# Kernel tuning notes

Measured on AMD Instinct MI355X. Metric: run time of the kernel, lower is better.

## Reference

```python
import jax, jax.numpy as jnp
import numpy as np

N_NODES = 100000
N_EDGES = 3200000
D_IN, D_HID, D_OUT = 128, 128, 128


def setup_inputs() -> dict:
    key = jax.random.key(0)
    ks = jax.random.split(key, 8)
    x = jax.random.normal(ks[0], (N_NODES, D_IN), dtype=jnp.float32)
    edge_index = jax.random.randint(ks[1], (2, N_EDGES), 0, N_NODES, dtype=jnp.int64)
    def lin(k, din, dout):
        # glorot-ish init for GCNConv weight
        s = 1.0 / np.sqrt(din)
        return jax.random.uniform(k, (din, dout), jnp.float32, -s, s)
    W0 = lin(ks[2], D_IN, D_HID)
    b0 = jnp.zeros((D_HID,), jnp.float32)
    W1 = lin(ks[3], D_HID, D_HID)
    b1 = jnp.zeros((D_HID,), jnp.float32)
    W2 = lin(ks[4], D_HID, D_OUT)
    b2 = jnp.zeros((D_OUT,), jnp.float32)
    return {"x": x, "edge_index": edge_index, "W0": W0, "b0": b0,
            "W1": W1, "b1": b1, "W2": W2, "b2": b2}


def _gcn_norm(edge_index, n_nodes):
    # PyG gcn_norm with self-loops: deg over target index, sym normalization
    loop = jnp.arange(n_nodes, dtype=edge_index.dtype)
    src = jnp.concatenate([edge_index[0], loop])
    dst = jnp.concatenate([edge_index[1], loop])
    deg = jax.ops.segment_sum(jnp.ones_like(dst, dtype=jnp.float32), dst,
                              num_segments=n_nodes)
    dinv = jnp.where(deg > 0, jax.lax.rsqrt(deg), 0.0)
    norm = dinv[src] * dinv[dst]  # [E + N]
    return src, dst, norm


def _gcn_conv(h, src, dst, norm, W, b, n_nodes):
    h = h @ W                                   # [N, dout] transform first
    msg = h[src] * norm[:, None]                # gather + scale
    out = jax.ops.segment_sum(msg, dst, num_segments=n_nodes)  # scatter-add
    return out + b


def reference(x, edge_index, W0, b0, W1, b1, W2, b2):
    n = x.shape[0]
    src, dst, norm = _gcn_norm(edge_index, n)
    # layer 0
    h = jax.nn.relu(_gcn_conv(x, src, dst, norm, W0, b0, n))
    # residual middle layer (dropout is identity in eval mode)
    h = jax.nn.relu(_gcn_conv(h, src, dst, norm, W1, b1, n) + h)
    # output layer
    return _gcn_conv(h, src, dst, norm, W2, b2, n)
```

## Files before the change

### kernel.cpp

```cpp
#include <hip/hip_runtime.h>
#include <hip/hip_fp16.h>

#define D 128
typedef unsigned long long ull;
typedef _Float16 half8 __attribute__((ext_vector_type(8)));
typedef _Float16 half4v __attribute__((ext_vector_type(4)));
typedef float f32x4 __attribute__((ext_vector_type(4)));

#define KPOS(k4) (((k4) & ~31) + ((((k4) & 15) >> 2) << 3) + ((((k4) >> 4) & 1) << 2))

__global__ void k_zero_int(int* p, int n) {
  int i = blockIdx.x * blockDim.x + threadIdx.x;
  if (i < n) p[i] = 0;
}

__global__ void k_deg_count(const int* __restrict__ ei, int* __restrict__ deg, int E) {
  int e = blockIdx.x * blockDim.x + threadIdx.x;
  if (e < E) atomicAdd(&deg[ei[E + e]], 1);
}

__global__ void k_scan_part(const int* __restrict__ deg, int* __restrict__ part, int n) {
  __shared__ int sd[256];
  int base = blockIdx.x * 2048 + threadIdx.x * 8;
  int s = 0;
#pragma unroll
  for (int k = 0; k < 8; k++) {
    int idx = base + k;
    if (idx < n) s += deg[idx];
  }
  sd[threadIdx.x] = s;
  __syncthreads();
  for (int off = 128; off > 0; off >>= 1) {
    if (threadIdx.x < off) sd[threadIdx.x] += sd[threadIdx.x + off];
    __syncthreads();
  }
  if (threadIdx.x == 0) part[blockIdx.x] = sd[0];
}

__global__ void k_scan_offsets(int* __restrict__ part, int nparts,
                               int* __restrict__ rowptr, int n) {
  __shared__ int sd[256];
  int v = (threadIdx.x < nparts) ? part[threadIdx.x] : 0;
  sd[threadIdx.x] = v;
  __syncthreads();
  for (int off = 1; off < 256; off <<= 1) {
    int t = (threadIdx.x >= off) ? sd[threadIdx.x - off] : 0;
    __syncthreads();
    sd[threadIdx.x] += t;
    __syncthreads();
  }
  if (threadIdx.x < nparts) part[threadIdx.x] = sd[threadIdx.x] - v;
  if (threadIdx.x == 0) rowptr[n] = sd[255];
}

__global__ void k_scan_final(const int* __restrict__ deg, const int* __restrict__ part,
                             int* __restrict__ rowptr, int n) {
  __shared__ int sd[256];
  int base = blockIdx.x * 2048 + threadIdx.x * 8;
  int loc[8];
  int s = 0;
#pragma unroll
  for (int k = 0; k < 8; k++) {
    int idx = base + k;
    loc[k] = (idx < n) ? deg[idx] : 0;
    s += loc[k];
  }
  sd[threadIdx.x] = s;
  __syncthreads();
  for (int off = 1; off < 256; off <<= 1) {
    int t = (threadIdx.x >= off) ? sd[threadIdx.x - off] : 0;
    __syncthreads();
    sd[threadIdx.x] += t;
    __syncthreads();
  }
  int run = part[blockIdx.x] + sd[threadIdx.x] - s;
#pragma unroll
  for (int k = 0; k < 8; k++) {
    int idx = base + k;
    if (idx < n) {
      rowptr[idx] = run;
      run += loc[k];
    }
  }
}

__global__ void k_dinv_cursor(const int* __restrict__ rowptr, float* __restrict__ dinv,
                              int* __restrict__ cursor, int n) {
  int i = blockIdx.x * blockDim.x + threadIdx.x;
  if (i < n) {
    int r0 = rowptr[i], r1 = rowptr[i + 1];
    dinv[i] = rsqrtf((float)(r1 - r0) + 1.0f);
    cursor[i] = r0;
  }
}

__global__ void k_csr_fill_b(const int* __restrict__ ei, int* __restrict__ cursor,
                             int* __restrict__ csr, int E, int lo, int hi) {
  int e = blockIdx.x * blockDim.x + threadIdx.x;
  if (e >= E) return;
  int d = __builtin_nontemporal_load(&ei[E + e]);
  if (d < lo || d >= hi) return;
  int s = __builtin_nontemporal_load(&ei[e]);
  int pos = atomicAdd(&cursor[d], 1);
  csr[pos] = s;
}

template <int HALF_IN>
__launch_bounds__(256, 2)
__global__ void k_gemm_mfma(const void* __restrict__ Av, const float* __restrict__ W,
                            const float* __restrict__ dinv, __half* __restrict__ Th, int n) {
  __shared__ _Float16 Al[128 * 136];
  __shared__ _Float16 Bl[128 * 136];
  const int tid = threadIdx.x;
  const int row0 = blockIdx.x * 128;

  if (HALF_IN) {
    const _Float16* A = (const _Float16*)Av;
    for (int i = tid; i < 2048; i += 256) {
      int r = i >> 4;
      int k8 = (i & 15) << 3;
      half8 v = {0, 0, 0, 0, 0, 0, 0, 0};
      if (row0 + r < n) v = *(const half8*)&A[(size_t)(row0 + r) * D + k8];
      *(half4v*)&Al[r * 136 + KPOS(k8)]     = (half4v){v[0], v[1], v[2], v[3]};
      *(half4v*)&Al[r * 136 + KPOS(k8 + 4)] = (half4v){v[4], v[5], v[6], v[7]};
    }
  } else {
    const float* A = (const float*)Av;
    for (int i = tid; i < 4096; i += 256) {
      int r = i >> 5;
      int k4 = (i & 31) << 2;
      float4 v = make_float4(0.f, 0.f, 0.f, 0.f);
      if (row0 + r < n) v = ((const float4*)A)[(size_t)(row0 + r) * 32 + (i & 31)];
      *(half4v*)&Al[r * 136 + KPOS(k4)] =
          (half4v){(_Float16)v.x, (_Float16)v.y, (_Float16)v.z, (_Float16)v.w};
    }
  }
  for (int i = tid; i < 4096; i += 256) {
    int c = i & 127;
    int k4 = (i >> 7) << 2;
    float w0 = W[(k4 + 0) * D + c];
    float w1 = W[(k4 + 1) * D + c];
    float w2 = W[(k4 + 2) * D + c];
    float w3 = W[(k4 + 3) * D + c];
    *(half4v*)&Bl[c * 136 + KPOS(k4)] =
        (half4v){(_Float16)w0, (_Float16)w1, (_Float16)w2, (_Float16)w3};
  }
  __syncthreads();

  const int w = tid >> 6;
  const int lane = tid & 63;
  const int g = lane >> 4;
  const int q = lane & 15;

  f32x4 acc[2][8];
#pragma unroll
  for (int mt = 0; mt < 2; mt++)
#pragma unroll
    for (int nt = 0; nt < 8; nt++) acc[mt][nt] = (f32x4){0.f, 0.f, 0.f, 0.f};

#pragma unroll
  for (int kt = 0; kt < 4; kt++) {
    half8 a[2], b[8];
#pragma unroll
    for (int mt = 0; mt < 2; mt++)
      a[mt] = *(const half8*)&Al[(w * 32 + mt * 16 + q) * 136 + kt * 32 + g * 8];
#pragma unroll
    for (int nt = 0; nt < 8; nt++)
      b[nt] = *(const half8*)&Bl[(nt * 16 + q) * 136 + kt * 32 + g * 8];
#pragma unroll
    for (int mt = 0; mt < 2; mt++)
#pragma unroll
      for (int nt = 0; nt < 8; nt++)
        acc[mt][nt] = __builtin_amdgcn_mfma_f32_16x16x32_f16(a[mt], b[nt], acc[mt][nt], 0, 0, 0);
  }

#pragma unroll
  for (int mt = 0; mt < 2; mt++) {
    int baseRow = row0 + w * 32 + mt * 16 + g * 4;
    float dv[4];
#pragma unroll
    for (int r = 0; r < 4; r++) dv[r] = (baseRow + r < n) ? dinv[baseRow + r] : 0.f;
#pragma unroll
    for (int nt = 0; nt < 8; nt++) {
      int col = nt * 16 + q;
#pragma unroll
      for (int r = 0; r < 4; r++) {
        int gr = baseRow + r;
        if (gr < n) Th[(size_t)gr * D + col] = (__half)(acc[mt][nt][r] * dv[r]);
      }
    }
  }
}

template <int MODE>
__launch_bounds__(256)
__global__ void k_aggregate(const int* __restrict__ rowptr, const int* __restrict__ csr,
                            const float* __restrict__ dinv, const __half* __restrict__ th,
                            const float* __restrict__ b, const __half* __restrict__ resh,
                            __half* __restrict__ outh, float* __restrict__ outf, int n) {
  int node = blockIdx.x * 16 + (threadIdx.x >> 4);
  if (node >= n) return;
  const int l16 = threadIdx.x & 15;

  int beg = rowptr[node];
  int end = rowptr[node + 1];
  float dd = dinv[node];

  const float4* t4 = (const float4*)th;

  float a0, a1, a2, a3, a4, a5, a6, a7;
  {
    float4 raw = t4[(size_t)node * 16 + l16];
    const __half2* hp = (const __half2*)&raw;
    float2 f0 = __half22float2(hp[0]);
    float2 f1 = __half22float2(hp[1]);
    float2 f2 = __half22float2(hp[2]);
    float2 f3 = __half22float2(hp[3]);
    a0 = f0.x; a1 = f0.y; a2 = f1.x; a3 = f1.y;
    a4 = f2.x; a5 = f2.y; a6 = f3.x; a7 = f3.y;
  }

#define ACC_ROW(raw)                                  \
  {                                                   \
    const __half2* hp = (const __half2*)&(raw);       \
    float2 f0 = __half22float2(hp[0]);                \
    float2 f1 = __half22float2(hp[1]);                \
    float2 f2 = __half22float2(hp[2]);                \
    float2 f3 = __half22float2(hp[3]);                \
    a0 += f0.x; a1 += f0.y; a2 += f1.x; a3 += f1.y;   \
    a4 += f2.x; a5 += f2.y; a6 += f3.x; a7 += f3.y;   \
  }

  int j = beg;
  for (; j + 8 <= end; j += 8) {
    float4 r0, r1, r2, r3, r4, r5, r6, r7;
    {
      int s0 = __builtin_nontemporal_load(&csr[j + 0]);
      int s1 = __builtin_nontemporal_load(&csr[j + 1]);
      int s2 = __builtin_nontemporal_load(&csr[j + 2]);
      int s3 = __builtin_nontemporal_load(&csr[j + 3]);
      int s4 = __builtin_nontemporal_load(&csr[j + 4]);
      int s5 = __builtin_nontemporal_load(&csr[j + 5]);
      int s6 = __builtin_nontemporal_load(&csr[j + 6]);
      int s7 = __builtin_nontemporal_load(&csr[j + 7]);
      r0 = t4[(size_t)(unsigned)s0 * 16 + l16];
      r1 = t4[(size_t)(unsigned)s1 * 16 + l16];
      r2 = t4[(size_t)(unsigned)s2 * 16 + l16];
      r3 = t4[(size_t)(unsigned)s3 * 16 + l16];
      r4 = t4[(size_t)(unsigned)s4 * 16 + l16];
      r5 = t4[(size_t)(unsigned)s5 * 16 + l16];
      r6 = t4[(size_t)(unsigned)s6 * 16 + l16];
      r7 = t4[(size_t)(unsigned)s7 * 16 + l16];
    }
    ACC_ROW(r0) ACC_ROW(r1) ACC_ROW(r2) ACC_ROW(r3)
    ACC_ROW(r4) ACC_ROW(r5) ACC_ROW(r6) ACC_ROW(r7)
  }
  for (; j + 4 <= end; j += 4) {
    int s0 = __builtin_nontemporal_load(&csr[j + 0]);
    int s1 = __builtin_nontemporal_load(&csr[j + 1]);
    int s2 = __builtin_nontemporal_load(&csr[j + 2]);
    int s3 = __builtin_nontemporal_load(&csr[j + 3]);
    float4 r0 = t4[(size_t)(unsigned)s0 * 16 + l16];
    float4 r1 = t4[(size_t)(unsigned)s1 * 16 + l16];
    float4 r2 = t4[(size_t)(unsigned)s2 * 16 + l16];
    float4 r3 = t4[(size_t)(unsigned)s3 * 16 + l16];
    ACC_ROW(r0) ACC_ROW(r1) ACC_ROW(r2) ACC_ROW(r3)
  }
  for (; j < end; ++j) {
    int s = __builtin_nontemporal_load(&csr[j]);
    float4 r = t4[(size_t)(unsigned)s * 16 + l16];
    ACC_ROW(r)
  }
#undef ACC_ROW

  const float4* b4 = (const float4*)b;
  float4 bb0 = b4[l16 * 2];
  float4 bb1 = b4[l16 * 2 + 1];
  float o0 = fmaf(a0, dd, bb0.x), o1 = fmaf(a1, dd, bb0.y);
  float o2 = fmaf(a2, dd, bb0.z), o3 = fmaf(a3, dd, bb0.w);
  float o4 = fmaf(a4, dd, bb1.x), o5 = fmaf(a5, dd, bb1.y);
  float o6 = fmaf(a6, dd, bb1.z), o7 = fmaf(a7, dd, bb1.w);

  if (MODE == 1) {
    float4 raw = ((const float4*)resh)[(size_t)node * 16 + l16];
    const __half2* hp = (const __half2*)&raw;
    float2 f0 = __half22float2(hp[0]);
    float2 f1 = __half22float2(hp[1]);
    float2 f2 = __half22float2(hp[2]);
    float2 f3 = __half22float2(hp[3]);
    o0 += f0.x; o1 += f0.y; o2 += f1.x; o3 += f1.y;
    o4 += f2.x; o5 += f2.y; o6 += f3.x; o7 += f3.y;
  }
  if (MODE == 0 || MODE == 1) {
    o0 = fmaxf(o0, 0.f); o1 = fmaxf(o1, 0.f); o2 = fmaxf(o2, 0.f); o3 = fmaxf(o3, 0.f);
    o4 = fmaxf(o4, 0.f); o5 = fmaxf(o5, 0.f); o6 = fmaxf(o6, 0.f); o7 = fmaxf(o7, 0.f);
    union { __half2 h[4]; float4 f; } pk;
    pk.h[0] = __floats2half2_rn(o0, o1);
    pk.h[1] = __floats2half2_rn(o2, o3);
    pk.h[2] = __floats2half2_rn(o4, o5);
    pk.h[3] = __floats2half2_rn(o6, o7);
    ((float4*)outh)[(size_t)node * 16 + l16] = pk.f;
  } else {
    ((float4*)outf)[(size_t)node * 32 + l16 * 2] = make_float4(o0, o1, o2, o3);
    ((float4*)outf)[(size_t)node * 32 + l16 * 2 + 1] = make_float4(o4, o5, o6, o7);
  }
}

extern "C" void kernel_launch(void* const* d_in, const int* in_sizes, int n_in,
                              void* d_out, int out_size, void* d_ws, size_t ws_size,
                              hipStream_t stream) {
  const float* x  = (const float*)d_in[0];
  const int*   ei = (const int*)d_in[1];
  const float* W0 = (const float*)d_in[2];
  const float* b0 = (const float*)d_in[3];
  const float* W1 = (const float*)d_in[4];
  const float* b1 = (const float*)d_in[5];
  const float* W2 = (const float*)d_in[6];
  const float* b2 = (const float*)d_in[7];
  float* out = (float*)d_out;

  const int N = in_sizes[0] / D;
  const int E = in_sizes[1] / 2;

  char* wsb = (char*)d_ws;
  auto alloc = [&](size_t bytes) {
    char* p = wsb;
    wsb += ((bytes + 255) & ~(size_t)255);
    return p;
  };
  int*    rowptr = (int*)alloc((N + 1) * 4);
  int*    cursor = (int*)alloc(N * 4);
  int*    part   = (int*)alloc(256 * 4);
  float*  dinv   = (float*)alloc(N * 4);
  int*    csr    = (int*)alloc((size_t)E * 4);
  __half* th     = (__half*)alloc((size_t)N * D * 2);
  __half* g1h    = (__half*)alloc((size_t)N * D * 2);
  __half* g2h    = (__half*)alloc((size_t)N * D * 2);

  dim3 b256(256);
  int gN   = (N + 255) / 256;
  int gE   = (E + 255) / 256;
  int gGem = (N + 127) / 128;
  int gAgg = (N + 15) / 16;
  int nparts = (N + 2047) / 2048;

  int* deg = cursor;
  k_zero_int<<<gN, b256, 0, stream>>>(deg, N);
  k_deg_count<<<gE, b256, 0, stream>>>(ei, deg, E);
  k_scan_part<<<nparts, b256, 0, stream>>>(deg, part, N);
  k_scan_offsets<<<1, b256, 0, stream>>>(part, nparts, rowptr, N);
  k_scan_final<<<nparts, b256, 0, stream>>>(deg, part, rowptr, N);
  k_dinv_cursor<<<gN, b256, 0, stream>>>(rowptr, dinv, cursor, N);
  const int NB = 4;
  int bsz = (N + NB - 1) / NB;
  for (int b = 0; b < NB; b++) {
    int lo = b * bsz;
    int hi = lo + bsz;
    if (hi > N) hi = N;
    k_csr_fill_b<<<gE, b256, 0, stream>>>(ei, cursor, csr, E, lo, hi);
  }

  k_gemm_mfma<0><<<gGem, b256, 0, stream>>>(x, W0, dinv, th, N);
  k_aggregate<0><<<gAgg, b256, 0, stream>>>(rowptr, csr, dinv, th, b0, nullptr, g1h, nullptr, N);

  k_gemm_mfma<1><<<gGem, b256, 0, stream>>>(g1h, W1, dinv, th, N);
  k_aggregate<1><<<gAgg, b256, 0, stream>>>(rowptr, csr, dinv, th, b1, g1h, g2h, nullptr, N);

  k_gemm_mfma<1><<<gGem, b256, 0, stream>>>(g2h, W2, dinv, th, N);
  k_aggregate<2><<<gAgg, b256, 0, stream>>>(rowptr, csr, dinv, th, b2, nullptr, nullptr, out, N);
}
```

Baseline: 814.2 us.

## Privatize degree counts and fuse bucketed CSR fill into one launch

Degree counting now spreads atomics across 8 private copies of the degree array, chosen by block index, then reduces them in a separate pass, to cut same-address atomic contention. The four sequential bucketed CSR-fill launches become one persistent-style launch in which each block handles one of 8 destination buckets over a slice of edges. That removes launch gaps and lets the buckets run concurrently, while each bucket still confines its atomics to a narrower range of cursor addresses. The cost is an extra 8N-int buffer with its zeroing and reduction passes, and the edge list is still read once per bucket, now 8 times instead of 4.

```diff
diff --git a/kernel.cpp b/kernel.cpp
--- a/kernel.cpp
+++ b/kernel.cpp
@@ -14,9 +14,21 @@
   if (i < n) p[i] = 0;
 }
 
-__global__ void k_deg_count(const int* __restrict__ ei, int* __restrict__ deg, int E) {
+__global__ void k_deg_count8(const int* __restrict__ ei, int* __restrict__ deg8,
+                             int E, int N) {
   int e = blockIdx.x * blockDim.x + threadIdx.x;
-  if (e < E) atomicAdd(&deg[ei[E + e]], 1);
+  if (e >= E) return;
+  int d = __builtin_nontemporal_load(&ei[E + e]);
+  atomicAdd(&deg8[(blockIdx.x & 7) * N + d], 1);
+}
+
+__global__ void k_deg_reduce(const int* __restrict__ deg8, int* __restrict__ deg, int N) {
+  int i = blockIdx.x * blockDim.x + threadIdx.x;
+  if (i >= N) return;
+  int s = 0;
+#pragma unroll
+  for (int c = 0; c < 8; c++) s += deg8[c * N + i];
+  deg[i] = s;
 }
 
 __global__ void k_scan_part(const int* __restrict__ deg, int* __restrict__ part, int n) {
@@ -94,15 +106,24 @@
   }
 }
 
-__global__ void k_csr_fill_b(const int* __restrict__ ei, int* __restrict__ cursor,
-                             int* __restrict__ csr, int E, int lo, int hi) {
-  int e = blockIdx.x * blockDim.x + threadIdx.x;
-  if (e >= E) return;
-  int d = __builtin_nontemporal_load(&ei[E + e]);
-  if (d < lo || d >= hi) return;
-  int s = __builtin_nontemporal_load(&ei[e]);
-  int pos = atomicAdd(&cursor[d], 1);
-  csr[pos] = s;
+__global__ void k_csr_fill_x(const int* __restrict__ ei, int* __restrict__ cursor,
+                             int* __restrict__ csr, int E, int bsz) {
+  const int bucket = blockIdx.x & 7;
+  const int slice = blockIdx.x >> 3;
+  const int nsl = gridDim.x >> 3;
+  const int lo = bucket * bsz;
+  const int chunk = (E + nsl - 1) / nsl;
+  const int start = slice * chunk;
+  int endE = start + chunk;
+  if (endE > E) endE = E;
+  for (int e = start + threadIdx.x; e < endE; e += 256) {
+    int d = __builtin_nontemporal_load(&ei[E + e]);
+    if ((unsigned)(d - lo) < (unsigned)bsz) {
+      int s = __builtin_nontemporal_load(&ei[e]);
+      int pos = atomicAdd(&cursor[d], 1);
+      csr[pos] = s;
+    }
+  }
 }
 
 template <int HALF_IN>
@@ -332,6 +353,7 @@
   int*    cursor = (int*)alloc(N * 4);
   int*    part   = (int*)alloc(256 * 4);
   float*  dinv   = (float*)alloc(N * 4);
+  int*    deg8   = (int*)alloc((size_t)8 * N * 4);
   int*    csr    = (int*)alloc((size_t)E * 4);
   __half* th     = (__half*)alloc((size_t)N * D * 2);
   __half* g1h    = (__half*)alloc((size_t)N * D * 2);
@@ -339,26 +361,22 @@
 
   dim3 b256(256);
   int gN   = (N + 255) / 256;
+  int gN8  = (8 * N + 255) / 256;
   int gE   = (E + 255) / 256;
   int gGem = (N + 127) / 128;
   int gAgg = (N + 15) / 16;
   int nparts = (N + 2047) / 2048;
 
   int* deg = cursor;
-  k_zero_int<<<gN, b256, 0, stream>>>(deg, N);
-  k_deg_count<<<gE, b256, 0, stream>>>(ei, deg, E);
+  k_zero_int<<<gN8, b256, 0, stream>>>(deg8, 8 * N);
+  k_deg_count8<<<gE, b256, 0, stream>>>(ei, deg8, E, N);
+  k_deg_reduce<<<gN, b256, 0, stream>>>(deg8, deg, N);
   k_scan_part<<<nparts, b256, 0, stream>>>(deg, part, N);
   k_scan_offsets<<<1, b256, 0, stream>>>(part, nparts, rowptr, N);
   k_scan_final<<<nparts, b256, 0, stream>>>(deg, part, rowptr, N);
   k_dinv_cursor<<<gN, b256, 0, stream>>>(rowptr, dinv, cursor, N);
-  const int NB = 4;
-  int bsz = (N + NB - 1) / NB;
-  for (int b = 0; b < NB; b++) {
-    int lo = b * bsz;
-    int hi = lo + bsz;
-    if (hi > N) hi = N;
-    k_csr_fill_b<<<gE, b256, 0, stream>>>(ei, cursor, csr, E, lo, hi);
-  }
+  int bsz = (N + 7) / 8;
+  k_csr_fill_x<<<8 * 256, b256, 0, stream>>>(ei, cursor, csr, E, bsz);
 
   k_gemm_mfma<0><<<gGem, b256, 0, stream>>>(x, W0, dinv, th, N);
   k_aggregate<0><<<gAgg, b256, 0, stream>>>(rowptr, csr, dinv, th, b0, nullptr, g1h, nullptr, N);
```

Measured after the change: 746.3 us. 8.3% less time.

## Build CSR via two-level bucket sort with shared-memory atomics

Applied to the files above, without the earlier changes.

Replaces global-atomic degree counting and the four-pass filtered CSR fill with a bucketed counting sort. Edges are first histogrammed per tile into 512-node buckets, scattered into a bucket-ordered edge buffer, then each bucket computes degrees and fills CSR using shared-memory atomics. This is meant to remove the contended global atomics and the four repeated full reads of the edge list. In exchange it writes and reads an extra 8-byte-per-edge intermediate buffer and adds several kernel launches. Bucket count must stay at most 256 for the single-block scan, which holds for this node count.

```diff
diff --git a/kernel.cpp b/kernel.cpp
--- a/kernel.cpp
+++ b/kernel.cpp
@@ -2,6 +2,7 @@
 #include <hip/hip_fp16.h>
 
 #define D 128
+#define TILE 16384
 typedef unsigned long long ull;
 typedef _Float16 half8 __attribute__((ext_vector_type(8)));
 typedef _Float16 half4v __attribute__((ext_vector_type(4)));
@@ -9,24 +10,97 @@
 
 #define KPOS(k4) (((k4) & ~31) + ((((k4) & 15) >> 2) << 3) + ((((k4) >> 4) & 1) << 2))
 
-__global__ void k_zero_int(int* p, int n) {
-  int i = blockIdx.x * blockDim.x + threadIdx.x;
-  if (i < n) p[i] = 0;
-}
-
-__global__ void k_deg_count(const int* __restrict__ ei, int* __restrict__ deg, int E) {
-  int e = blockIdx.x * blockDim.x + threadIdx.x;
-  if (e < E) atomicAdd(&deg[ei[E + e]], 1);
-}
-
-__global__ void k_scan_part(const int* __restrict__ deg, int* __restrict__ part, int n) {
+__global__ void k_cnt_tiles(const int* __restrict__ ei_dst, int* __restrict__ cnt,
+                            int E, int ntiles, int nb) {
+  __shared__ int h[256];
+  for (int i = threadIdx.x; i < nb; i += 256) h[i] = 0;
+  __syncthreads();
+  const int t = blockIdx.x;
+  const int start = t * TILE;
+  int end = start + TILE;
+  if (end > E) end = E;
+  for (int i = start + threadIdx.x; i < end; i += 256)
+    atomicAdd(&h[__builtin_nontemporal_load(&ei_dst[i]) >> 9], 1);
+  __syncthreads();
+  for (int b = threadIdx.x; b < nb; b += 256)
+    cnt[(size_t)b * ntiles + t] = h[b];
+}
+
+__global__ void k_tile_scan(const int* __restrict__ cnt, int* __restrict__ off,
+                            int nb, int ntiles) {
   __shared__ int sd[256];
-  int base = blockIdx.x * 2048 + threadIdx.x * 8;
+  int total = 0;
+  if (threadIdx.x < nb) {
+    const int* row = cnt + (size_t)threadIdx.x * ntiles;
+    for (int t = 0; t < ntiles; t++) total += row[t];
+  }
+  sd[threadIdx.x] = total;
+  __syncthreads();
+  for (int o = 1; o < 256; o <<= 1) {
+    int v = (threadIdx.x >= o) ? sd[threadIdx.x - o] : 0;
+    __syncthreads();
+    sd[threadIdx.x] += v;
+    __syncthreads();
+  }
+  int base = sd[threadIdx.x] - total;
+  if (threadIdx.x < nb) {
+    const int* row = cnt + (size_t)threadIdx.x * ntiles;
+    int* orow = off + (size_t)threadIdx.x * ntiles;
+    int run = base;
+    for (int t = 0; t < ntiles; t++) { orow[t] = run; run += row[t]; }
+  }
+}
+
+__global__ void k_scatter_bucket(const int* __restrict__ ei, const int* __restrict__ off,
+                                 ull* __restrict__ ebb, int E, int ntiles, int nb) {
+  __shared__ int h[256];
+  __shared__ int base[256];
+  const int t = blockIdx.x;
+  for (int i = threadIdx.x; i < nb; i += 256) {
+    h[i] = 0;
+    base[i] = off[(size_t)i * ntiles + t];
+  }
+  __syncthreads();
+  const int start = t * TILE;
+  int end = start + TILE;
+  if (end > E) end = E;
+  for (int i = start + threadIdx.x; i < end; i += 256) {
+    int d = __builtin_nontemporal_load(&ei[E + i]);
+    int s = __builtin_nontemporal_load(&ei[i]);
+    int b = d >> 9;
+    int r = atomicAdd(&h[b], 1);
+    ebb[(size_t)base[b] + r] = (ull)(unsigned)s | ((ull)(unsigned)d << 32);
+  }
+}
+
+__global__ void k_deg_bucket(const ull* __restrict__ ebb, const int* __restrict__ off,
+                             int* __restrict__ deg, int E, int ntiles, int nb, int N) {
+  __shared__ int cnt[512];
+  const int b = blockIdx.x;
+  for (int i = threadIdx.x; i < 512; i += 256) cnt[i] = 0;
+  const int lo = off[(size_t)b * ntiles];
+  const int hi = (b + 1 < nb) ? off[(size_t)(b + 1) * ntiles] : E;
+  __syncthreads();
+  for (int i = lo + threadIdx.x; i < hi; i += 256) {
+    ull q = __builtin_nontemporal_load(&ebb[i]);
+    atomicAdd(&cnt[(int)(q >> 32) - (b << 9)], 1);
+  }
+  __syncthreads();
+  for (int i = threadIdx.x; i < 512; i += 256) {
+    int v = (b << 9) + i;
+    if (v < N) deg[v] = cnt[i];
+  }
+}
+
+template <int ITEMS>
+__global__ void k_scan_part(const int* __restrict__ v, int* __restrict__ part, int n) {
+  __shared__ int sd[256];
+  int base = blockIdx.x * (256 * ITEMS) + threadIdx.x * ITEMS;
   int s = 0;
 #pragma unroll
-  for (int k = 0; k < 8; k++) {
+  for (int k = 0; k < ITEMS; k++) {
     int idx = base + k;
-    if (idx < n) s += deg[idx];
+    if (idx < n) s += v[idx];
   }
   sd[threadIdx.x] = s;
   __syncthreads();
@@ -38,7 +112,7 @@
 }
 
 __global__ void k_scan_offsets(int* __restrict__ part, int nparts,
-                               int* __restrict__ rowptr, int n) {
+                               int* __restrict__ outp, int n) {
   __shared__ int sd[256];
   int v = (threadIdx.x < nparts) ? part[threadIdx.x] : 0;
   sd[threadIdx.x] = v;
@@ -50,19 +124,20 @@
     __syncthreads();
   }
   if (threadIdx.x < nparts) part[threadIdx.x] = sd[threadIdx.x] - v;
-  if (threadIdx.x == 0) rowptr[n] = sd[255];
-}
-
-__global__ void k_scan_final(const int* __restrict__ deg, const int* __restrict__ part,
-                             int* __restrict__ rowptr, int n) {
+  if (threadIdx.x == 0) outp[n] = sd[255];
+}
+
+template <int ITEMS>
+__global__ void k_scan_final(const int* __restrict__ v, const int* __restrict__ part,
+                             int* __restrict__ outp, int n) {
   __shared__ int sd[256];
-  int base = blockIdx.x * 2048 + threadIdx.x * 8;
-  int loc[8];
+  int base = blockIdx.x * (256 * ITEMS) + threadIdx.x * ITEMS;
+  int loc[ITEMS];
   int s = 0;
 #pragma unroll
-  for (int k = 0; k < 8; k++) {
+  for (int k = 0; k < ITEMS; k++) {
     int idx = base + k;
-    loc[k] = (idx < n) ? deg[idx] : 0;
+    loc[k] = (idx < n) ? v[idx] : 0;
     s += loc[k];
   }
   sd[threadIdx.x] = s;
@@ -75,34 +150,39 @@
   }
   int run = part[blockIdx.x] + sd[threadIdx.x] - s;
 #pragma unroll
-  for (int k = 0; k < 8; k++) {
+  for (int k = 0; k < ITEMS; k++) {
     int idx = base + k;
     if (idx < n) {
-      rowptr[idx] = run;
+      outp[idx] = run;
       run += loc[k];
     }
   }
 }
 
-__global__ void k_dinv_cursor(const int* __restrict__ rowptr, float* __restrict__ dinv,
-                              int* __restrict__ cursor, int n) {
+__global__ void k_dinv(const int* __restrict__ deg, float* __restrict__ dinv, int n) {
   int i = blockIdx.x * blockDim.x + threadIdx.x;
-  if (i < n) {
-    int r0 = rowptr[i], r1 = rowptr[i + 1];
-    dinv[i] = rsqrtf((float)(r1 - r0) + 1.0f);
-    cursor[i] = r0;
-  }
-}
-
-__global__ void k_csr_fill_b(const int* __restrict__ ei, int* __restrict__ cursor,
-                             int* __restrict__ csr, int E, int lo, int hi) {
-  int e = blockIdx.x * blockDim.x + threadIdx.x;
-  if (e >= E) return;
-  int d = __builtin_nontemporal_load(&ei[E + e]);
-  if (d < lo || d >= hi) return;
-  int s = __builtin_nontemporal_load(&ei[e]);
-  int pos = atomicAdd(&cursor[d], 1);
-  csr[pos] = s;
+  if (i < n) dinv[i] = rsqrtf((float)deg[i] + 1.0f);
+}
+
+__global__ void k_fill_bucket(const ull* __restrict__ ebb, const int* __restrict__ off,
+                              const int* __restrict__ rowptr, int* __restrict__ csr,
+                              int E, int ntiles, int nb, int N) {
+  __shared__ int cur[512];
+  const int b = blockIdx.x;
+  for (int i = threadIdx.x; i < 512; i += 256) {
+    int v = (b << 9) + i;
+    cur[i] = (v < N) ? rowptr[v] : 0;
+  }
+  const int lo = off[(size_t)b * ntiles];
+  const int hi = (b + 1 < nb) ? off[(size_t)(b + 1) * ntiles] : E;
+  __syncthreads();
+  for (int i = lo + threadIdx.x; i < hi; i += 256) {
+    ull q = __builtin_nontemporal_load(&ebb[i]);
+    int s = (int)(unsigned)q;
+    int dl = (int)(q >> 32) - (b << 9);
+    int pos = atomicAdd(&cur[dl], 1);
+    csr[pos] = s;
+  }
 }
 
 template <int HALF_IN>
@@ -322,6 +402,9 @@
   const int N = in_sizes[0] / D;
   const int E = in_sizes[1] / 2;
 
+  const int ntiles = (E + TILE - 1) / TILE;
+  const int nb = (N + 511) >> 9;
+
   char* wsb = (char*)d_ws;
   auto alloc = [&](size_t bytes) {
     char* p = wsb;
@@ -329,9 +412,12 @@
     return p;
   };
   int*    rowptr = (int*)alloc((N + 1) * 4);
-  int*    cursor = (int*)alloc(N * 4);
+  int*    deg    = (int*)alloc(N * 4);
   int*    part   = (int*)alloc(256 * 4);
   float*  dinv   = (float*)alloc(N * 4);
+  int*    cnt    = (int*)alloc((size_t)nb * ntiles * 4);
+  int*    off    = (int*)alloc((size_t)nb * ntiles * 4);
+  ull*    ebb    = (ull*)alloc((size_t)E * 8);
   int*    csr    = (int*)alloc((size_t)E * 4);
   __half* th     = (__half*)alloc((size_t)N * D * 2);
   __half* g1h    = (__half*)alloc((size_t)N * D * 2);
@@ -339,26 +425,19 @@
 
   dim3 b256(256);
   int gN   = (N + 255) / 256;
-  int gE   = (E + 255) / 256;
   int gGem = (N + 127) / 128;
   int gAgg = (N + 15) / 16;
-  int nparts = (N + 2047) / 2048;
-
-  int* deg = cursor;
-  k_zero_int<<<gN, b256, 0, stream>>>(deg, N);
-  k_deg_count<<<gE, b256, 0, stream>>>(ei, deg, E);
-  k_scan_part<<<nparts, b256, 0, stream>>>(deg, part, N);
-  k_scan_offsets<<<1, b256, 0, stream>>>(part, nparts, rowptr, N);
-  k_scan_final<<<nparts, b256, 0, stream>>>(deg, part, rowptr, N);
-  k_dinv_cursor<<<gN, b256, 0, stream>>>(rowptr, dinv, cursor, N);
-  const int NB = 4;
-  int bsz = (N + NB - 1) / NB;
-  for (int b = 0; b < NB; b++) {
-    int lo = b * bsz;
-    int hi = lo + bsz;
-    if (hi > N) hi = N;
-    k_csr_fill_b<<<gE, b256, 0, stream>>>(ei, cursor, csr, E, lo, hi);
-  }
+  int np1  = (N + 2047) / 2048;
+
+  k_cnt_tiles<<<ntiles, b256, 0, stream>>>(ei + E, cnt, E, ntiles, nb);
+  k_tile_scan<<<1, b256, 0, stream>>>(cnt, off, nb, ntiles);
+  k_scatter_bucket<<<ntiles, b256, 0, stream>>>(ei, off, ebb, E, ntiles, nb);
+  k_deg_bucket<<<nb, b256, 0, stream>>>(ebb, off, deg, E, ntiles, nb, N);
+  k_scan_part<8><<<np1, b256, 0, stream>>>(deg, part, N);
+  k_scan_offsets<<<1, b256, 0, stream>>>(part, np1, rowptr, N);
+  k_scan_final<8><<<np1, b256, 0, stream>>>(deg, part, rowptr, N);
+  k_dinv<<<gN, b256, 0, stream>>>(deg, dinv, N);
+  k_fill_bucket<<<nb, b256, 0, stream>>>(ebb, off, rowptr, csr, E, ntiles, nb, N);
 
   k_gemm_mfma<0><<<gGem, b256, 0, stream>>>(x, W0, dinv, th, N);
   k_aggregate<0><<<gAgg, b256, 0, stream>>>(rowptr, csr, dinv, th, b0, nullptr, g1h, nullptr, N);
```

Result: faster. 665.6 us (-18.2%).
